# Optimization experiments

Hardware: AMD Instinct MI355X
Metric: run time of the kernel (lower is better)

Reference implementation:

```python
import jax, jax.numpy as jnp
import numpy as np

E = 8        # num_experts
TOP_K = 2    # num_experts_per_tok
AUX_COEFF = 0.01


def _grok_ffn(x, g, u, d):
    # down(gelu(gate(x)) * up(x)); torch F.gelu default is exact (erf)
    return (jax.nn.gelu(x @ g.T, approximate=False) * (x @ u.T)) @ d.T


def setup_inputs() -> dict:
    key = jax.random.key(0)
    ks = jax.random.split(key, 8)
    B, T, D, H = 4, 4096, 1024, 2816
    s = 0.02
    return {
        "x": jax.random.normal(ks[0], (B, T, D), dtype=jnp.float32),
        "gate_w": jax.random.normal(ks[1], (E, D), dtype=jnp.float32) * 0.01,
        "wg": jax.random.normal(ks[2], (E, H, D), dtype=jnp.float32) * s,
        "wu": jax.random.normal(ks[3], (E, H, D), dtype=jnp.float32) * s,
        "wd": jax.random.normal(ks[4], (E, D, H), dtype=jnp.float32) * s,
        "sg": jax.random.normal(ks[5], (H, D), dtype=jnp.float32) * s,
        "su": jax.random.normal(ks[6], (H, D), dtype=jnp.float32) * s,
        "sd": jax.random.normal(ks[7], (D, H), dtype=jnp.float32) * s,
    }


def reference(x, gate_w, wg, wu, wd, sg, su, sd):
    B, T, D = x.shape
    xf = x.reshape(B * T, D)  # (N, D)

    # ---- router ----
    logits = (xf @ gate_w.T).astype(jnp.float32)          # (N, E)
    top_v, top_i = jax.lax.top_k(logits, TOP_K)           # (N, K)
    expert_weights = jax.nn.softmax(top_v, axis=-1)       # (N, K)
    gates = jax.nn.softmax(logits, axis=-1)               # (N, E)
    f = jax.nn.one_hot(top_i[:, 0], E, dtype=jnp.float32).mean(axis=0)
    P = gates.mean(axis=0)
    aux_loss = AUX_COEFF * E * (f * P).sum()

    # combine weight per (token, expert): sum_k w[t,k] * [idx[t,k]==e]
    onehot = jax.nn.one_hot(top_i, E, dtype=jnp.float32)  # (N, K, E)
    combine = (expert_weights[..., None] * onehot).sum(axis=1)  # (N, E)

    # ---- expert compute (loop over small fixed expert count) ----
    out = jnp.zeros_like(xf)
    for e in range(E):
        out = out + combine[:, e:e + 1] * _grok_ffn(xf, wg[e], wu[e], wd[e])

    out = out.reshape(B, T, D)
    out = out + _grok_ffn(x, sg, su, sd)  # shared expert
    return out, aux_loss
```

## Files before the change

kernel.cpp:

```cpp
#include <hip/hip_runtime.h>
#include <cstdint>

#define NE 8
#define NEX 9
#define NTOK 16384
#define DDIM 1024
#define HDIM 2816

typedef unsigned short u16;
typedef __attribute__((ext_vector_type(8))) short short8;
typedef __attribute__((ext_vector_type(4))) float f32x4;

__device__ __forceinline__ u16 f2bf(float f) {
  uint32_t u = __builtin_bit_cast(uint32_t, f);
  u += 0x7FFFu + ((u >> 16) & 1u);
  return (u16)(u >> 16);
}

__device__ __forceinline__ float wave_reduce_sum(float v) {
  for (int off = 32; off > 0; off >>= 1) v += __shfl_xor(v, off, 64);
  return v;
}

#define GLOAD16(gsrc, ldst)                                                   \
  __builtin_amdgcn_global_load_lds(                                           \
      (const __attribute__((address_space(1))) unsigned int*)(gsrc),          \
      (__attribute__((address_space(3))) unsigned int*)(ldst), 16, 0, 0)

__device__ __forceinline__ void xcd_map(int NT, int MT, int* nt, int* mt) {
  int lin = blockIdx.y * NT + blockIdx.x;
  int nwg = NT * MT;
  int q = nwg >> 3, r = nwg & 7;
  int xcd = lin & 7, idx = lin >> 3;
  int nl = (xcd < r) ? (xcd * (q + 1) + idx) : (r * (q + 1) + (xcd - r) * q + idx);
  *nt = nl / MT;
  *mt = nl % MT;
}

__global__ void init_kernel(int* cnt, float* Pacc, float* fcnt) {
  int t = threadIdx.x;
  if (t < NEX) cnt[t] = (t == 8) ? NTOK : 0;
  if (t < NE) { Pacc[t] = 0.f; fcnt[t] = 0.f; }
}

struct CvtArgs {
  const float* src[7];
  u16* dst[7];
  long long cum[8];
};

__global__ void convert_kernel(CvtArgs a) {
  long long stride = (long long)gridDim.x * blockDim.x;
  long long total = a.cum[7];
  for (long long g = (long long)blockIdx.x * blockDim.x + threadIdx.x; g < total; g += stride) {
    int s = 0;
    while (g >= a.cum[s + 1]) s++;
    long long off = (g - a.cum[s]) * 4;
    float4 v = *reinterpret_cast<const float4*>(a.src[s] + off);
    union { u16 u[4]; uint2 w; } o;
    o.u[0] = f2bf(v.x); o.u[1] = f2bf(v.y); o.u[2] = f2bf(v.z); o.u[3] = f2bf(v.w);
    *reinterpret_cast<uint2*>(a.dst[s] + off) = o.w;
  }
}

__global__ __launch_bounds__(256) void router_kernel(
    const float* __restrict__ x, const float* __restrict__ gw,
    int* __restrict__ tok, float* __restrict__ wtl,
    int* __restrict__ cnt, float* __restrict__ Pacc, float* __restrict__ fcnt) {
  int lane = threadIdx.x & 63;
  int wv = threadIdx.x >> 6;
  __shared__ float red[4][16];
  float pP[NE], pF[NE];
#pragma unroll
  for (int e = 0; e < NE; e++) { pP[e] = 0.f; pF[e] = 0.f; }
  int t0 = blockIdx.x * 16 + wv * 4;
  for (int ti = 0; ti < 4; ti++) {
    int t = t0 + ti;
    float part[NE];
#pragma unroll
    for (int e = 0; e < NE; e++) part[e] = 0.f;
    const float* xp = x + (size_t)t * DDIM;
#pragma unroll
    for (int j = 0; j < 16; j++) {
      float xv = xp[lane + j * 64];
#pragma unroll
      for (int e = 0; e < NE; e++) part[e] += xv * gw[e * DDIM + lane + j * 64];
    }
#pragma unroll
    for (int e = 0; e < NE; e++) part[e] = wave_reduce_sum(part[e]);
    if (lane == 0) {
      float v0 = -1e30f, v1 = -1e30f; int i0 = 0, i1 = 0;
#pragma unroll
      for (int e = 0; e < NE; e++) {
        float v = part[e];
        if (v > v0) { v1 = v0; i1 = i0; v0 = v; i0 = e; }
        else if (v > v1) { v1 = v; i1 = e; }
      }
      float e1 = expf(v1 - v0);
      float w0 = 1.f / (1.f + e1);
      float w1 = e1 * w0;
      float s = 0.f, g[NE];
#pragma unroll
      for (int e = 0; e < NE; e++) { g[e] = expf(part[e] - v0); s += g[e]; }
      float inv = 1.f / s;
#pragma unroll
      for (int e = 0; e < NE; e++) pP[e] += g[e] * inv;
      pF[i0] += 1.f;
      int p0 = atomicAdd(&cnt[i0], 1);
      tok[i0 * NTOK + p0] = t; wtl[i0 * NTOK + p0] = w0;
      int p1 = atomicAdd(&cnt[i1], 1);
      tok[i1 * NTOK + p1] = t; wtl[i1 * NTOK + p1] = w1;
      tok[8 * NTOK + t] = t; wtl[8 * NTOK + t] = 1.f;
    }
  }
  if (lane == 0) {
#pragma unroll
    for (int e = 0; e < NE; e++) { red[wv][e] = pP[e]; red[wv][e + 8] = pF[e]; }
  }
  __syncthreads();
  if (threadIdx.x < 16) {
    float s = red[0][threadIdx.x] + red[1][threadIdx.x] + red[2][threadIdx.x] + red[3][threadIdx.x];
    if (threadIdx.x < 8) atomicAdd(&Pacc[threadIdx.x], s);
    else atomicAdd(&fcnt[threadIdx.x - 8], s);
  }
}

__global__ void finalize_router(const int* cnt, int* offs, const float* Pacc,
                                const float* fcnt, float* out_aux) {
  if (threadIdx.x == 0 && blockIdx.x == 0) {
    int p = NTOK;
    for (int e = 0; e < NE; e++) { offs[e] = p; p += cnt[e]; }
    offs[8] = 0;
    float aux = 0.f;
    for (int e = 0; e < NE; e++)
      aux += (fcnt[e] * (1.f / NTOK)) * (Pacc[e] * (1.f / NTOK));
    *out_aux = 0.01f * 8.f * aux;
  }
}


template<bool WB>
__global__ __launch_bounds__(256, 2) void pass1_kernel(
    const u16* __restrict__ xbf, const void* __restrict__ WGall,
    const void* __restrict__ WUall, const void* __restrict__ SG,
    const void* __restrict__ SU, const int* __restrict__ tok,
    const int* __restrict__ cnt, const int* __restrict__ offs,
    u16* __restrict__ Abuf, int e0, int ab_off) {
  int nt, mt;
  xcd_map(gridDim.x, gridDim.y, &nt, &mt);
  int e = e0 + blockIdx.z;
  int Me = cnt[e];
  if (mt * 128 >= Me) return;
  int base = offs[e];
  int ab = (ab_off < 0) ? base : ab_off;

  __shared__ u16 lX[128 * 64];
  __shared__ u16 lG[128 * 64];
  __shared__ u16 lU[128 * 64];

  int tid = threadIdx.x, lane = tid & 63, wv = tid >> 6;
  int wr = wv >> 1, wc = wv & 1;
  size_t wst = (size_t)HDIM * DDIM;
  int swsrc = ((lane & 7) ^ (lane >> 3)) * 8;

  const u16* gx[4];
#pragma unroll
  for (int q = 0; q < 4; q++) {
    int r = (wv * 4 + q) * 8 + (lane >> 3);
    int gm = mt * 128 + r;
    int tk = (gm < Me) ? tok[e * NTOK + gm] : 0;
    gx[q] = xbf + (size_t)tk * DDIM + swsrc;
  }

  const u16 *gg[4], *gu[4];
  const float *pg0 = nullptr, *pu0 = nullptr;
  int st_r0 = 0, st_chunk = 0, st_win = 0;
  if constexpr (WB) {
    const u16* G = (e == 8) ? (const u16*)SG : (const u16*)WGall + (size_t)e * wst;
    const u16* U = (e == 8) ? (const u16*)SU : (const u16*)WUall + (size_t)e * wst;
#pragma unroll
    for (int q = 0; q < 4; q++) {
      int r = (wv * 4 + q) * 8 + (lane >> 3);
      gg[q] = G + (size_t)(nt * 128 + r) * DDIM + swsrc;
      gu[q] = U + (size_t)(nt * 128 + r) * DDIM + swsrc;
    }
  } else {
    const float* G = (e == 8) ? (const float*)SG : (const float*)WGall + (size_t)e * wst;
    const float* U = (e == 8) ? (const float*)SU : (const float*)WUall + (size_t)e * wst;
    st_r0 = wv * 32 + (lane >> 4);
    int c0 = (lane & 15) * 4;
    st_chunk = c0 >> 3; st_win = c0 & 7;
    pg0 = G + (size_t)(nt * 128 + st_r0) * DDIM + c0;
    pu0 = U + (size_t)(nt * 128 + st_r0) * DDIM + c0;
  }

  f32x4 accG[4][4] = {};
  f32x4 accU[4][4] = {};

  for (int kt = 0; kt < DDIM / 64; kt++) {
    __syncthreads();
    int ko = kt * 64;
#pragma unroll
    for (int q = 0; q < 4; q++)
      GLOAD16(gx[q] + ko, lX + (wv * 4 + q) * 512);
    if constexpr (WB) {
#pragma unroll
      for (int q = 0; q < 4; q++) {
        int ldsoff = (wv * 4 + q) * 512;
        GLOAD16(gg[q] + ko, lG + ldsoff);
        GLOAD16(gu[q] + ko, lU + ldsoff);
      }
    } else {
#pragma unroll
      for (int q = 0; q < 8; q++) {
        int row = st_r0 + q * 4;
        int pc = (((st_chunk ^ (row & 7)) << 3) | st_win);
        float4 vg = *reinterpret_cast<const float4*>(pg0 + ko + q * 4 * DDIM);
        float4 vu = *reinterpret_cast<const float4*>(pu0 + ko + q * 4 * DDIM);
        union { u16 h[4]; uint2 w; } og, ou;
        og.h[0] = f2bf(vg.x); og.h[1] = f2bf(vg.y); og.h[2] = f2bf(vg.z); og.h[3] = f2bf(vg.w);
        ou.h[0] = f2bf(vu.x); ou.h[1] = f2bf(vu.y); ou.h[2] = f2bf(vu.z); ou.h[3] = f2bf(vu.w);
        *reinterpret_cast<uint2*>(lG + row * 64 + pc) = og.w;
        *reinterpret_cast<uint2*>(lU + row * 64 + pc) = ou.w;
      }
    }
    asm volatile("s_waitcnt vmcnt(0)" ::: "memory");
    __syncthreads();

    __builtin_amdgcn_s_setprio(1);
#pragma unroll
    for (int kk = 0; kk < 2; kk++) {
      int kbs = (((kk * 4 + (lane >> 4)) ^ (lane & 7))) * 8;
      short8 af[4];
#pragma unroll
      for (int m = 0; m < 4; m++) {
        int row = wr * 64 + m * 16 + (lane & 15);
        af[m] = *reinterpret_cast<const short8*>(lX + row * 64 + kbs);
      }
#pragma unroll
      for (int n = 0; n < 4; n++) {
        int hr = wc * 64 + n * 16 + (lane & 15);
        short8 bg = *reinterpret_cast<const short8*>(lG + hr * 64 + kbs);
        short8 bu = *reinterpret_cast<const short8*>(lU + hr * 64 + kbs);
#pragma unroll
        for (int m = 0; m < 4; m++) {
          accG[m][n] = __builtin_amdgcn_mfma_f32_16x16x32_bf16(af[m], bg, accG[m][n], 0, 0, 0);
          accU[m][n] = __builtin_amdgcn_mfma_f32_16x16x32_bf16(af[m], bu, accU[m][n], 0, 0, 0);
        }
      }
    }
    __builtin_amdgcn_s_setprio(0);
  }

  int rsub = (lane >> 4) * 4, csub = lane & 15;
#pragma unroll
  for (int m = 0; m < 4; m++) {
#pragma unroll
    for (int i = 0; i < 4; i++) {
      int row = wr * 64 + m * 16 + rsub + i;
      int gm = mt * 128 + row;
      if (gm < Me) {
        size_t rb = (size_t)(base + gm - ab) * HDIM + nt * 128;
#pragma unroll
        for (int n = 0; n < 4; n++) {
          float hg = accG[m][n][i];
          float hu = accU[m][n][i];
          float a = 0.5f * hg * (1.f + erff(hg * 0.70710678118f)) * hu;
          Abuf[rb + wc * 64 + n * 16 + csub] = f2bf(a);
        }
      }
    }
  }
}

template<bool WB>
__global__ __launch_bounds__(256, 2) void pass2_kernel(
    const u16* __restrict__ Abuf, const void* __restrict__ WDall,
    const void* __restrict__ SD, const int* __restrict__ tok,
    const float* __restrict__ wtl, const int* __restrict__ cnt,
    const int* __restrict__ offs, float* __restrict__ out, int e0, int ab_off) {
  int nt, mt;
  xcd_map(gridDim.x, gridDim.y, &nt, &mt);
  int e = e0 + blockIdx.z;
  int Me = cnt[e];
  if (mt * 128 >= Me) return;
  int base = offs[e];
  int ab = (ab_off < 0) ? base : ab_off;
  size_t wst = (size_t)HDIM * DDIM;

  __shared__ u16 lA[128 * 64];
  __shared__ u16 lB[128 * 64];

  int tid = threadIdx.x, lane = tid & 63, wv = tid >> 6;
  int wr = wv >> 1, wc = wv & 1;
  int swsrc = ((lane & 7) ^ (lane >> 3)) * 8;

  const u16* ga[4];
#pragma unroll
  for (int q = 0; q < 4; q++) {
    int r = (wv * 4 + q) * 8 + (lane >> 3);
    int slot = base + mt * 128 + r - ab;
    ga[q] = Abuf + (size_t)slot * HDIM + swsrc;
  }

  const u16* gb[4];
  const float* pd0 = nullptr;
  int st_r0 = 0, st_chunk = 0, st_win = 0;
  if constexpr (WB) {
    const u16* D = (e == 8) ? (const u16*)SD : (const u16*)WDall + (size_t)e * wst;
#pragma unroll
    for (int q = 0; q < 4; q++) {
      int r = (wv * 4 + q) * 8 + (lane >> 3);
      gb[q] = D + (size_t)(nt * 128 + r) * HDIM + swsrc;
    }
  } else {
    const float* D = (e == 8) ? (const float*)SD : (const float*)WDall + (size_t)e * wst;
    st_r0 = wv * 32 + (lane >> 4);
    int c0 = (lane & 15) * 4;
    st_chunk = c0 >> 3; st_win = c0 & 7;
    pd0 = D + (size_t)(nt * 128 + st_r0) * HDIM + c0;
  }

  f32x4 acc[4][4] = {};

  for (int kt = 0; kt < HDIM / 64; kt++) {
    __syncthreads();
    int ko = kt * 64;
#pragma unroll
    for (int q = 0; q < 4; q++)
      GLOAD16(ga[q] + ko, lA + (wv * 4 + q) * 512);
    if constexpr (WB) {
#pragma unroll
      for (int q = 0; q < 4; q++)
        GLOAD16(gb[q] + ko, lB + (wv * 4 + q) * 512);
    } else {
#pragma unroll
      for (int q = 0; q < 8; q++) {
        int row = st_r0 + q * 4;
        int pc = (((st_chunk ^ (row & 7)) << 3) | st_win);
        float4 vd = *reinterpret_cast<const float4*>(pd0 + ko + q * 4 * HDIM);
        union { u16 h[4]; uint2 w; } od;
        od.h[0] = f2bf(vd.x); od.h[1] = f2bf(vd.y); od.h[2] = f2bf(vd.z); od.h[3] = f2bf(vd.w);
        *reinterpret_cast<uint2*>(lB + row * 64 + pc) = od.w;
      }
    }
    asm volatile("s_waitcnt vmcnt(0)" ::: "memory");
    __syncthreads();

    __builtin_amdgcn_s_setprio(1);
#pragma unroll
    for (int kk = 0; kk < 2; kk++) {
      int kbs = (((kk * 4 + (lane >> 4)) ^ (lane & 7))) * 8;
      short8 af[4];
#pragma unroll
      for (int m = 0; m < 4; m++) {
        int row = wr * 64 + m * 16 + (lane & 15);
        af[m] = *reinterpret_cast<const short8*>(lA + row * 64 + kbs);
      }
#pragma unroll
      for (int n = 0; n < 4; n++) {
        int dr = wc * 64 + n * 16 + (lane & 15);
        short8 bd = *reinterpret_cast<const short8*>(lB + dr * 64 + kbs);
#pragma unroll
        for (int m = 0; m < 4; m++)
          acc[m][n] = __builtin_amdgcn_mfma_f32_16x16x32_bf16(af[m], bd, acc[m][n], 0, 0, 0);
      }
    }
    __builtin_amdgcn_s_setprio(0);
  }

  int rsub = (lane >> 4) * 4, csub = lane & 15;
#pragma unroll
  for (int m = 0; m < 4; m++) {
#pragma unroll
    for (int i = 0; i < 4; i++) {
      int row = wr * 64 + m * 16 + rsub + i;
      int gm = mt * 128 + row;
      if (gm < Me) {
        int t = tok[e * NTOK + gm];
        float w = (e == 8) ? 1.f : wtl[e * NTOK + gm];
        size_t ob = (size_t)t * DDIM + nt * 128;
#pragma unroll
        for (int n = 0; n < 4; n++) {
          float v = w * acc[m][n][i];
          int c = wc * 64 + n * 16 + csub;
          if (e == 8) out[ob + c] = out[ob + c] + v;
          else atomicAdd(&out[ob + c], v);
        }
      }
    }
  }
}

extern "C" void kernel_launch(void* const* d_in, const int* in_sizes, int n_in,
                              void* d_out, int out_size, void* d_ws, size_t ws_size,
                              hipStream_t stream) {
  const float* x  = (const float*)d_in[0];
  const float* gw = (const float*)d_in[1];
  const float* wg = (const float*)d_in[2];
  const float* wu = (const float*)d_in[3];
  const float* wd = (const float*)d_in[4];
  const float* sg = (const float*)d_in[5];
  const float* su = (const float*)d_in[6];
  const float* sd = (const float*)d_in[7];
  float* out = (float*)d_out;

  bool tierF = ws_size >= 327000000ULL;
  bool tierE = !tierF && ws_size >= 223000000ULL;

  char* ws = (char*)d_ws;
  size_t o = 0;
  auto alloc = [&](size_t bytes) -> void* {
    void* p = ws + o;
    o = (o + bytes + 255) & ~(size_t)255;
    return p;
  };
  u16* xbf = (u16*)alloc((size_t)NTOK * DDIM * 2);
  u16 *wgbf = nullptr, *wubf = nullptr, *sgbf = nullptr, *subf = nullptr;
  u16 *wdbf = nullptr, *sdbf = nullptr;
  if (tierF) {
    wgbf = (u16*)alloc((size_t)NE * HDIM * DDIM * 2);
    wubf = (u16*)alloc((size_t)NE * HDIM * DDIM * 2);
    sgbf = (u16*)alloc((size_t)HDIM * DDIM * 2);
    subf = (u16*)alloc((size_t)HDIM * DDIM * 2);
    wdbf = wgbf;
    sdbf = wgbf + (size_t)NE * DDIM * HDIM;
  }
  size_t abuf_rows = (tierF || tierE) ? ((size_t)2 * NTOK + 128) : ((size_t)NTOK + 128);
  u16* Abuf = (u16*)alloc(abuf_rows * HDIM * 2);
  int*   tok  = (int*)alloc((size_t)NEX * NTOK * 4);
  float* wtl  = (float*)alloc((size_t)NEX * NTOK * 4);
  int*   cnt  = (int*)alloc(64);
  int*   offs = (int*)alloc(64);
  float* Pacc = (float*)alloc(64);
  float* fcnt = (float*)alloc(64);

  hipMemsetAsync(d_out, 0, (size_t)out_size * 4, stream);
  init_kernel<<<1, 64, 0, stream>>>(cnt, Pacc, fcnt);

  {
    CvtArgs ca;
    long long sizes4[7];
    int nsrc = 0;
    ca.src[nsrc] = x; ca.dst[nsrc] = xbf; sizes4[nsrc] = (long long)NTOK * DDIM / 4; nsrc++;
    if (tierF) {
      ca.src[nsrc] = wg; ca.dst[nsrc] = wgbf; sizes4[nsrc] = (long long)NE * HDIM * DDIM / 4; nsrc++;
      ca.src[nsrc] = wu; ca.dst[nsrc] = wubf; sizes4[nsrc] = (long long)NE * HDIM * DDIM / 4; nsrc++;
      ca.src[nsrc] = sg; ca.dst[nsrc] = sgbf; sizes4[nsrc] = (long long)HDIM * DDIM / 4; nsrc++;
      ca.src[nsrc] = su; ca.dst[nsrc] = subf; sizes4[nsrc] = (long long)HDIM * DDIM / 4; nsrc++;
    }
    ca.cum[0] = 0;
    for (int i = 0; i < 7; i++)
      ca.cum[i + 1] = ca.cum[i] + (i < nsrc ? sizes4[i] : 0);
    convert_kernel<<<4096, 256, 0, stream>>>(ca);
  }

  router_kernel<<<NTOK / 16, 256, 0, stream>>>(x, gw, tok, wtl, cnt, Pacc, fcnt);
  finalize_router<<<1, 64, 0, stream>>>(cnt, offs, Pacc, fcnt, out + (out_size - 1));

  if (tierF) {
    pass1_kernel<true><<<dim3(HDIM / 128, NTOK / 128, NE), 256, 0, stream>>>(
        xbf, wgbf, wubf, sgbf, subf, tok, cnt, offs, Abuf, 0, NTOK);
    {
      CvtArgs ca;
      ca.src[0] = wd; ca.dst[0] = wdbf;
      ca.src[1] = sd; ca.dst[1] = sdbf;
      long long s0 = (long long)NE * DDIM * HDIM / 4;
      long long s1 = (long long)DDIM * HDIM / 4;
      ca.cum[0] = 0; ca.cum[1] = s0; ca.cum[2] = s0 + s1;
      for (int i = 3; i <= 7; i++) ca.cum[i] = ca.cum[2];
      convert_kernel<<<4096, 256, 0, stream>>>(ca);
    }
    pass2_kernel<true><<<dim3(DDIM / 128, NTOK / 128, NE), 256, 0, stream>>>(
        Abuf, wdbf, sdbf, tok, wtl, cnt, offs, out, 0, NTOK);
    pass1_kernel<true><<<dim3(HDIM / 128, NTOK / 128, 1), 256, 0, stream>>>(
        xbf, wgbf, wubf, sgbf, subf, tok, cnt, offs, Abuf, 8, 0);
    pass2_kernel<true><<<dim3(DDIM / 128, NTOK / 128, 1), 256, 0, stream>>>(
        Abuf, wdbf, sdbf, tok, wtl, cnt, offs, out, 8, 0);
  } else if (tierE) {
    pass1_kernel<false><<<dim3(HDIM / 128, NTOK / 128, 1), 256, 0, stream>>>(
        xbf, wg, wu, sg, su, tok, cnt, offs, Abuf, 8, 0);
    pass2_kernel<false><<<dim3(DDIM / 128, NTOK / 128, 1), 256, 0, stream>>>(
        Abuf, wd, sd, tok, wtl, cnt, offs, out, 8, 0);
    pass1_kernel<false><<<dim3(HDIM / 128, NTOK / 128, NE), 256, 0, stream>>>(
        xbf, wg, wu, sg, su, tok, cnt, offs, Abuf, 0, NTOK);
    pass2_kernel<false><<<dim3(DDIM / 128, NTOK / 128, NE), 256, 0, stream>>>(
        Abuf, wd, sd, tok, wtl, cnt, offs, out, 0, NTOK);
  } else {
    for (int k = 0; k < NEX; k++) {
      int e = (k == 0) ? 8 : (k - 1);
      pass1_kernel<false><<<dim3(HDIM / 128, NTOK / 128, 1), 256, 0, stream>>>(
          xbf, wg, wu, sg, su, tok, cnt, offs, Abuf, e, -1);
      pass2_kernel<false><<<dim3(DDIM / 128, NTOK / 128, 1), 256, 0, stream>>>(
          Abuf, wd, sd, tok, wtl, cnt, offs, out, e, -1);
    }
  }
}
```

Measured before the change: 1.687 ms.

## Add double-buffered bf16 pass kernels with 256-row pass1 tiles

```diff
diff --git a/kernel.cpp b/kernel.cpp
--- a/kernel.cpp
+++ b/kernel.cpp
@@ -139,11 +139,225 @@
 }
 
 
-template<bool WB>
+
+__global__ __launch_bounds__(512, 2) void pass1p_kernel(
+    const u16* __restrict__ xbf, const u16* __restrict__ WGall,
+    const u16* __restrict__ WUall, const u16* __restrict__ SG,
+    const u16* __restrict__ SU, const int* __restrict__ tok,
+    const int* __restrict__ cnt, const int* __restrict__ offs,
+    u16* __restrict__ Abuf, int e0, int ab_off) {
+  int nt, mt;
+  xcd_map(gridDim.x, gridDim.y, &nt, &mt);
+  int e = e0 + blockIdx.z;
+  int Me = cnt[e];
+  if (mt * 256 >= Me) return;
+  int base = offs[e];
+
+  __shared__ u16 lX[2][256 * 64];
+  __shared__ u16 lG[2][128 * 64];
+  __shared__ u16 lU[2][128 * 64];
+
+  int tid = threadIdx.x, lane = tid & 63, wv = tid >> 6;
+  int wm = wv >> 1, wn = wv & 1;
+  size_t wst = (size_t)HDIM * DDIM;
+  int swsrc = ((lane & 7) ^ (lane >> 3)) * 8;
+
+  const u16* gx[4];
+#pragma unroll
+  for (int q = 0; q < 4; q++) {
+    int r = (wv * 4 + q) * 8 + (lane >> 3);
+    int gm = mt * 256 + r;
+    int tk = (gm < Me) ? tok[e * NTOK + gm] : 0;
+    gx[q] = xbf + (size_t)tk * DDIM + swsrc;
+  }
+  const u16* G = (e == 8) ? SG : WGall + (size_t)e * wst;
+  const u16* U = (e == 8) ? SU : WUall + (size_t)e * wst;
+  const u16 *gg[2], *gu[2];
+#pragma unroll
+  for (int q = 0; q < 2; q++) {
+    int r = (wv * 2 + q) * 8 + (lane >> 3);
+    gg[q] = G + (size_t)(nt * 128 + r) * DDIM + swsrc;
+    gu[q] = U + (size_t)(nt * 128 + r) * DDIM + swsrc;
+  }
+
+  f32x4 accG[4][4] = {};
+  f32x4 accU[4][4] = {};
+
+#pragma unroll
+  for (int q = 0; q < 4; q++) GLOAD16(gx[q], &lX[0][(wv * 4 + q) * 512]);
+#pragma unroll
+  for (int q = 0; q < 2; q++) {
+    GLOAD16(gg[q], &lG[0][(wv * 2 + q) * 512]);
+    GLOAD16(gu[q], &lU[0][(wv * 2 + q) * 512]);
+  }
+
+  for (int kt = 0; kt < DDIM / 64; kt++) {
+    int cur = kt & 1, nb = cur ^ 1;
+    int kon = (kt + 1 < DDIM / 64) ? (kt + 1) * 64 : 0;
+#pragma unroll
+    for (int q = 0; q < 4; q++) GLOAD16(gx[q] + kon, &lX[nb][(wv * 4 + q) * 512]);
+    asm volatile("s_waitcnt vmcnt(4)" ::: "memory");
+    __syncthreads();
+#pragma unroll
+    for (int kk = 0; kk < 2; kk++) {
+      if (kk == 1) {
+#pragma unroll
+        for (int q = 0; q < 2; q++) {
+          GLOAD16(gg[q] + kon, &lG[nb][(wv * 2 + q) * 512]);
+          GLOAD16(gu[q] + kon, &lU[nb][(wv * 2 + q) * 512]);
+        }
+      }
+      int kbs = ((kk * 4 + (lane >> 4)) ^ (lane & 7)) * 8;
+      short8 af[4];
+#pragma unroll
+      for (int m = 0; m < 4; m++) {
+        int row = wm * 64 + m * 16 + (lane & 15);
+        af[m] = *reinterpret_cast<const short8*>(&lX[cur][row * 64 + kbs]);
+      }
+      __builtin_amdgcn_s_setprio(1);
+#pragma unroll
+      for (int n = 0; n < 4; n++) {
+        int hr = wn * 64 + n * 16 + (lane & 15);
+        short8 bg = *reinterpret_cast<const short8*>(&lG[cur][hr * 64 + kbs]);
+        short8 bu = *reinterpret_cast<const short8*>(&lU[cur][hr * 64 + kbs]);
+#pragma unroll
+        for (int m = 0; m < 4; m++) {
+          accG[m][n] = __builtin_amdgcn_mfma_f32_16x16x32_bf16(af[m], bg, accG[m][n], 0, 0, 0);
+          accU[m][n] = __builtin_amdgcn_mfma_f32_16x16x32_bf16(af[m], bu, accU[m][n], 0, 0, 0);
+        }
+      }
+      __builtin_amdgcn_s_setprio(0);
+    }
+    __syncthreads();
+  }
+  asm volatile("s_waitcnt vmcnt(0)" ::: "memory");
+
+  int rsub = (lane >> 4) * 4, csub = lane & 15;
+#pragma unroll
+  for (int m = 0; m < 4; m++) {
+#pragma unroll
+    for (int i = 0; i < 4; i++) {
+      int row = wm * 64 + m * 16 + rsub + i;
+      int gm = mt * 256 + row;
+      if (gm < Me) {
+        size_t rb = (size_t)(base + gm - ab_off) * HDIM + nt * 128;
+#pragma unroll
+        for (int n = 0; n < 4; n++) {
+          float hg = accG[m][n][i];
+          float hu = accU[m][n][i];
+          float a = 0.5f * hg * (1.f + erff(hg * 0.70710678118f)) * hu;
+          Abuf[rb + wn * 64 + n * 16 + csub] = f2bf(a);
+        }
+      }
+    }
+  }
+}
+
+__global__ __launch_bounds__(256, 2) void pass2p_kernel(
+    const u16* __restrict__ Abuf, const u16* __restrict__ WDall,
+    const u16* __restrict__ SD, const int* __restrict__ tok,
+    const float* __restrict__ wtl, const int* __restrict__ cnt,
+    const int* __restrict__ offs, float* __restrict__ out, int e0, int ab_off) {
+  int nt, mt;
+  xcd_map(gridDim.x, gridDim.y, &nt, &mt);
+  int e = e0 + blockIdx.z;
+  int Me = cnt[e];
+  if (mt * 128 >= Me) return;
+  int base = offs[e];
+  size_t wst = (size_t)HDIM * DDIM;
+
+  __shared__ u16 lA[2][128 * 64];
+  __shared__ u16 lB[2][128 * 64];
+
+  int tid = threadIdx.x, lane = tid & 63, wv = tid >> 6;
+  int wr = wv >> 1, wc = wv & 1;
+  int swsrc = ((lane & 7) ^ (lane >> 3)) * 8;
+
+  const u16* ga[4];
+#pragma unroll
+  for (int q = 0; q < 4; q++) {
+    int r = (wv * 4 + q) * 8 + (lane >> 3);
+    int slot = base + mt * 128 + r - ab_off;
+    ga[q] = Abuf + (size_t)slot * HDIM + swsrc;
+  }
+  const u16* D = (e == 8) ? SD : WDall + (size_t)e * wst;
+  const u16* gb[4];
+#pragma unroll
+  for (int q = 0; q < 4; q++) {
+    int r = (wv * 4 + q) * 8 + (lane >> 3);
+    gb[q] = D + (size_t)(nt * 128 + r) * HDIM + swsrc;
+  }
+
+  f32x4 acc[4][4] = {};
+
+#pragma unroll
+  for (int q = 0; q < 4; q++) GLOAD16(ga[q], &lA[0][(wv * 4 + q) * 512]);
+#pragma unroll
+  for (int q = 0; q < 4; q++) GLOAD16(gb[q], &lB[0][(wv * 4 + q) * 512]);
+
+  for (int kt = 0; kt < HDIM / 64; kt++) {
+    int cur = kt & 1, nb = cur ^ 1;
+    int kon = (kt + 1 < HDIM / 64) ? (kt + 1) * 64 : 0;
+#pragma unroll
+    for (int q = 0; q < 4; q++) GLOAD16(ga[q] + kon, &lA[nb][(wv * 4 + q) * 512]);
+    asm volatile("s_waitcnt vmcnt(4)" ::: "memory");
+    __syncthreads();
+#pragma unroll
+    for (int kk = 0; kk < 2; kk++) {
+      if (kk == 1) {
+#pragma unroll
+        for (int q = 0; q < 4; q++) GLOAD16(gb[q] + kon, &lB[nb][(wv * 4 + q) * 512]);
+      }
+      int kbs = ((kk * 4 + (lane >> 4)) ^ (lane & 7)) * 8;
+      short8 af[4];
+#pragma unroll
+      for (int m = 0; m < 4; m++) {
+        int row = wr * 64 + m * 16 + (lane & 15);
+        af[m] = *reinterpret_cast<const short8*>(&lA[cur][row * 64 + kbs]);
+      }
+      __builtin_amdgcn_s_setprio(1);
+#pragma unroll
+      for (int n = 0; n < 4; n++) {
+        int dr = wc * 64 + n * 16 + (lane & 15);
+        short8 bd = *reinterpret_cast<const short8*>(&lB[cur][dr * 64 + kbs]);
+#pragma unroll
+        for (int m = 0; m < 4; m++)
+          acc[m][n] = __builtin_amdgcn_mfma_f32_16x16x32_bf16(af[m], bd, acc[m][n], 0, 0, 0);
+      }
+      __builtin_amdgcn_s_setprio(0);
+    }
+    __syncthreads();
+  }
+  asm volatile("s_waitcnt vmcnt(0)" ::: "memory");
+
+  int rsub = (lane >> 4) * 4, csub = lane & 15;
+#pragma unroll
+  for (int m = 0; m < 4; m++) {
+#pragma unroll
+    for (int i = 0; i < 4; i++) {
+      int row = wr * 64 + m * 16 + rsub + i;
+      int gm = mt * 128 + row;
+      if (gm < Me) {
+        int t = tok[e * NTOK + gm];
+        float w = (e == 8) ? 1.f : wtl[e * NTOK + gm];
+        size_t ob = (size_t)t * DDIM + nt * 128;
+#pragma unroll
+        for (int n = 0; n < 4; n++) {
+          float v = w * acc[m][n][i];
+          int c = wc * 64 + n * 16 + csub;
+          if (e == 8) out[ob + c] = out[ob + c] + v;
+          else atomicAdd(&out[ob + c], v);
+        }
+      }
+    }
+  }
+}
+
+
 __global__ __launch_bounds__(256, 2) void pass1_kernel(
-    const u16* __restrict__ xbf, const void* __restrict__ WGall,
-    const void* __restrict__ WUall, const void* __restrict__ SG,
-    const void* __restrict__ SU, const int* __restrict__ tok,
+    const u16* __restrict__ xbf, const float* __restrict__ WGall,
+    const float* __restrict__ WUall, const float* __restrict__ SG,
+    const float* __restrict__ SU, const int* __restrict__ tok,
     const int* __restrict__ cnt, const int* __restrict__ offs,
     u16* __restrict__ Abuf, int e0, int ab_off) {
   int nt, mt;
@@ -171,28 +385,13 @@
     int tk = (gm < Me) ? tok[e * NTOK + gm] : 0;
     gx[q] = xbf + (size_t)tk * DDIM + swsrc;
   }
-
-  const u16 *gg[4], *gu[4];
-  const float *pg0 = nullptr, *pu0 = nullptr;
-  int st_r0 = 0, st_chunk = 0, st_win = 0;
-  if constexpr (WB) {
-    const u16* G = (e == 8) ? (const u16*)SG : (const u16*)WGall + (size_t)e * wst;
-    const u16* U = (e == 8) ? (const u16*)SU : (const u16*)WUall + (size_t)e * wst;
-#pragma unroll
-    for (int q = 0; q < 4; q++) {
-      int r = (wv * 4 + q) * 8 + (lane >> 3);
-      gg[q] = G + (size_t)(nt * 128 + r) * DDIM + swsrc;
-      gu[q] = U + (size_t)(nt * 128 + r) * DDIM + swsrc;
-    }
-  } else {
-    const float* G = (e == 8) ? (const float*)SG : (const float*)WGall + (size_t)e * wst;
-    const float* U = (e == 8) ? (const float*)SU : (const float*)WUall + (size_t)e * wst;
-    st_r0 = wv * 32 + (lane >> 4);
-    int c0 = (lane & 15) * 4;
-    st_chunk = c0 >> 3; st_win = c0 & 7;
-    pg0 = G + (size_t)(nt * 128 + st_r0) * DDIM + c0;
-    pu0 = U + (size_t)(nt * 128 + st_r0) * DDIM + c0;
-  }
+  const float* G = (e == 8) ? SG : WGall + (size_t)e * wst;
+  const float* U = (e == 8) ? SU : WUall + (size_t)e * wst;
+  int st_r0 = wv * 32 + (lane >> 4);
+  int c0 = (lane & 15) * 4;
+  int st_chunk = c0 >> 3, st_win = c0 & 7;
+  const float* pg0 = G + (size_t)(nt * 128 + st_r0) * DDIM + c0;
+  const float* pu0 = U + (size_t)(nt * 128 + st_r0) * DDIM + c0;
 
   f32x4 accG[4][4] = {};
   f32x4 accU[4][4] = {};
@@ -203,26 +402,17 @@
 #pragma unroll
     for (int q = 0; q < 4; q++)
       GLOAD16(gx[q] + ko, lX + (wv * 4 + q) * 512);
-    if constexpr (WB) {
-#pragma unroll
-      for (int q = 0; q < 4; q++) {
-        int ldsoff = (wv * 4 + q) * 512;
-        GLOAD16(gg[q] + ko, lG + ldsoff);
-        GLOAD16(gu[q] + ko, lU + ldsoff);
-      }
-    } else {
-#pragma unroll
-      for (int q = 0; q < 8; q++) {
-        int row = st_r0 + q * 4;
-        int pc = (((st_chunk ^ (row & 7)) << 3) | st_win);
-        float4 vg = *reinterpret_cast<const float4*>(pg0 + ko + q * 4 * DDIM);
-        float4 vu = *reinterpret_cast<const float4*>(pu0 + ko + q * 4 * DDIM);
-        union { u16 h[4]; uint2 w; } og, ou;
-        og.h[0] = f2bf(vg.x); og.h[1] = f2bf(vg.y); og.h[2] = f2bf(vg.z); og.h[3] = f2bf(vg.w);
-        ou.h[0] = f2bf(vu.x); ou.h[1] = f2bf(vu.y); ou.h[2] = f2bf(vu.z); ou.h[3] = f2bf(vu.w);
-        *reinterpret_cast<uint2*>(lG + row * 64 + pc) = og.w;
-        *reinterpret_cast<uint2*>(lU + row * 64 + pc) = ou.w;
-      }
+#pragma unroll
+    for (int q = 0; q < 8; q++) {
+      int row = st_r0 + q * 4;
+      int pc = (((st_chunk ^ (row & 7)) << 3) | st_win);
+      float4 vg = *reinterpret_cast<const float4*>(pg0 + ko + q * 4 * DDIM);
+      float4 vu = *reinterpret_cast<const float4*>(pu0 + ko + q * 4 * DDIM);
+      union { u16 h[4]; uint2 w; } og, ou;
+      og.h[0] = f2bf(vg.x); og.h[1] = f2bf(vg.y); og.h[2] = f2bf(vg.z); og.h[3] = f2bf(vg.w);
+      ou.h[0] = f2bf(vu.x); ou.h[1] = f2bf(vu.y); ou.h[2] = f2bf(vu.z); ou.h[3] = f2bf(vu.w);
+      *reinterpret_cast<uint2*>(lG + row * 64 + pc) = og.w;
+      *reinterpret_cast<uint2*>(lU + row * 64 + pc) = ou.w;
     }
     asm volatile("s_waitcnt vmcnt(0)" ::: "memory");
     __syncthreads();
@@ -273,10 +463,9 @@
   }
 }
 
-template<bool WB>
 __global__ __launch_bounds__(256, 2) void pass2_kernel(
-    const u16* __restrict__ Abuf, const void* __restrict__ WDall,
-    const void* __restrict__ SD, const int* __restrict__ tok,
+    const u16* __restrict__ Abuf, const float* __restrict__ WDall,
+    const float* __restrict__ SD, const int* __restrict__ tok,
     const float* __restrict__ wtl, const int* __restrict__ cnt,
     const int* __restrict__ offs, float* __restrict__ out, int e0, int ab_off) {
   int nt, mt;
@@ -302,24 +491,11 @@
     int slot = base + mt * 128 + r - ab;
     ga[q] = Abuf + (size_t)slot * HDIM + swsrc;
   }
-
-  const u16* gb[4];
-  const float* pd0 = nullptr;
-  int st_r0 = 0, st_chunk = 0, st_win = 0;
-  if constexpr (WB) {
-    const u16* D = (e == 8) ? (const u16*)SD : (const u16*)WDall + (size_t)e * wst;
-#pragma unroll
-    for (int q = 0; q < 4; q++) {
-      int r = (wv * 4 + q) * 8 + (lane >> 3);
-      gb[q] = D + (size_t)(nt * 128 + r) * HDIM + swsrc;
-    }
-  } else {
-    const float* D = (e == 8) ? (const float*)SD : (const float*)WDall + (size_t)e * wst;
-    st_r0 = wv * 32 + (lane >> 4);
-    int c0 = (lane & 15) * 4;
-    st_chunk = c0 >> 3; st_win = c0 & 7;
-    pd0 = D + (size_t)(nt * 128 + st_r0) * HDIM + c0;
-  }
+  const float* D = (e == 8) ? SD : WDall + (size_t)e * wst;
+  int st_r0 = wv * 32 + (lane >> 4);
+  int c0 = (lane & 15) * 4;
+  int st_chunk = c0 >> 3, st_win = c0 & 7;
+  const float* pd0 = D + (size_t)(nt * 128 + st_r0) * HDIM + c0;
 
   f32x4 acc[4][4] = {};
 
@@ -329,20 +505,14 @@
 #pragma unroll
     for (int q = 0; q < 4; q++)
       GLOAD16(ga[q] + ko, lA + (wv * 4 + q) * 512);
-    if constexpr (WB) {
-#pragma unroll
-      for (int q = 0; q < 4; q++)
-        GLOAD16(gb[q] + ko, lB + (wv * 4 + q) * 512);
-    } else {
-#pragma unroll
-      for (int q = 0; q < 8; q++) {
-        int row = st_r0 + q * 4;
-        int pc = (((st_chunk ^ (row & 7)) << 3) | st_win);
-        float4 vd = *reinterpret_cast<const float4*>(pd0 + ko + q * 4 * HDIM);
-        union { u16 h[4]; uint2 w; } od;
-        od.h[0] = f2bf(vd.x); od.h[1] = f2bf(vd.y); od.h[2] = f2bf(vd.z); od.h[3] = f2bf(vd.w);
-        *reinterpret_cast<uint2*>(lB + row * 64 + pc) = od.w;
-      }
+#pragma unroll
+    for (int q = 0; q < 8; q++) {
+      int row = st_r0 + q * 4;
+      int pc = (((st_chunk ^ (row & 7)) << 3) | st_win);
+      float4 vd = *reinterpret_cast<const float4*>(pd0 + ko + q * 4 * HDIM);
+      union { u16 h[4]; uint2 w; } od;
+      od.h[0] = f2bf(vd.x); od.h[1] = f2bf(vd.y); od.h[2] = f2bf(vd.z); od.h[3] = f2bf(vd.w);
+      *reinterpret_cast<uint2*>(lB + row * 64 + pc) = od.w;
     }
     asm volatile("s_waitcnt vmcnt(0)" ::: "memory");
     __syncthreads();
@@ -426,7 +596,7 @@
     wdbf = wgbf;
     sdbf = wgbf + (size_t)NE * DDIM * HDIM;
   }
-  size_t abuf_rows = (tierF || tierE) ? ((size_t)2 * NTOK + 128) : ((size_t)NTOK + 128);
+  size_t abuf_rows = (tierF || tierE) ? ((size_t)2 * NTOK + 256) : ((size_t)NTOK + 256);
   u16* Abuf = (u16*)alloc(abuf_rows * HDIM * 2);
   int*   tok  = (int*)alloc((size_t)NEX * NTOK * 4);
   float* wtl  = (float*)alloc((size_t)NEX * NTOK * 4);
@@ -459,7 +629,7 @@
   finalize_router<<<1, 64, 0, stream>>>(cnt, offs, Pacc, fcnt, out + (out_size - 1));
 
   if (tierF) {
-    pass1_kernel<true><<<dim3(HDIM / 128, NTOK / 128, NE), 256, 0, stream>>>(
+    pass1p_kernel<<<dim3(HDIM / 128, NTOK / 256, NE), 512, 0, stream>>>(
         xbf, wgbf, wubf, sgbf, subf, tok, cnt, offs, Abuf, 0, NTOK);
     {
       CvtArgs ca;
@@ -471,27 +641,27 @@
       for (int i = 3; i <= 7; i++) ca.cum[i] = ca.cum[2];
       convert_kernel<<<4096, 256, 0, stream>>>(ca);
     }
-    pass2_kernel<true><<<dim3(DDIM / 128, NTOK / 128, NE), 256, 0, stream>>>(
+    pass2p_kernel<<<dim3(DDIM / 128, NTOK / 128, NE), 256, 0, stream>>>(
         Abuf, wdbf, sdbf, tok, wtl, cnt, offs, out, 0, NTOK);
-    pass1_kernel<true><<<dim3(HDIM / 128, NTOK / 128, 1), 256, 0, stream>>>(
+    pass1p_kernel<<<dim3(HDIM / 128, NTOK / 256, 1), 512, 0, stream>>>(
         xbf, wgbf, wubf, sgbf, subf, tok, cnt, offs, Abuf, 8, 0);
-    pass2_kernel<true><<<dim3(DDIM / 128, NTOK / 128, 1), 256, 0, stream>>>(
+    pass2p_kernel<<<dim3(DDIM / 128, NTOK / 128, 1), 256, 0, stream>>>(
         Abuf, wdbf, sdbf, tok, wtl, cnt, offs, out, 8, 0);
   } else if (tierE) {
-    pass1_kernel<false><<<dim3(HDIM / 128, NTOK / 128, 1), 256, 0, stream>>>(
+    pass1_kernel<<<dim3(HDIM / 128, NTOK / 128, 1), 256, 0, stream>>>(
         xbf, wg, wu, sg, su, tok, cnt, offs, Abuf, 8, 0);
-    pass2_kernel<false><<<dim3(DDIM / 128, NTOK / 128, 1), 256, 0, stream>>>(
+    pass2_kernel<<<dim3(DDIM / 128, NTOK / 128, 1), 256, 0, stream>>>(
         Abuf, wd, sd, tok, wtl, cnt, offs, out, 8, 0);
-    pass1_kernel<false><<<dim3(HDIM / 128, NTOK / 128, NE), 256, 0, stream>>>(
+    pass1_kernel<<<dim3(HDIM / 128, NTOK / 128, NE), 256, 0, stream>>>(
         xbf, wg, wu, sg, su, tok, cnt, offs, Abuf, 0, NTOK);
-    pass2_kernel<false><<<dim3(DDIM / 128, NTOK / 128, NE), 256, 0, stream>>>(
+    pass2_kernel<<<dim3(DDIM / 128, NTOK / 128, NE), 256, 0, stream>>>(
         Abuf, wd, sd, tok, wtl, cnt, offs, out, 0, NTOK);
   } else {
     for (int k = 0; k < NEX; k++) {
       int e = (k == 0) ? 8 : (k - 1);
-      pass1_kernel<false><<<dim3(HDIM / 128, NTOK / 128, 1), 256, 0, stream>>>(
+      pass1_kernel<<<dim3(HDIM / 128, NTOK / 128, 1), 256, 0, stream>>>(
           xbf, wg, wu, sg, su, tok, cnt, offs, Abuf, e, -1);
-      pass2_kernel<false><<<dim3(DDIM / 128, NTOK / 128, 1), 256, 0, stream>>>(
+      pass2_kernel<<<dim3(DDIM / 128, NTOK / 128, 1), 256, 0, stream>>>(
           Abuf, wd, sd, tok, wtl, cnt, offs, out, e, -1);
     }
   }
```

Result: slower. 2.102 ms (+24.6%).
